# Kernel optimization log

Measured on AMD Instinct MI355X. Metric: run time of the kernel, lower is better.

Reference implementation:

```python
import jax, jax.numpy as jnp
import numpy as np

B, S, R = 8192, 256, 8192  # gas cells, species, reactions


def setup_inputs() -> dict:
    key = jax.random.key(0)
    ks = jax.random.split(key, 10)
    abundances = jax.random.uniform(ks[0], (B, S), jnp.float32, 1e-12, 1.0)
    temperature = jax.random.uniform(ks[1], (B,), jnp.float32, 10.0, 300.0)
    cr_rate = jax.random.uniform(ks[2], (B,), jnp.float32, 0.1, 10.0)
    fuv_rate = jax.random.uniform(ks[3], (B,), jnp.float32, 0.1, 10.0)
    time = jnp.zeros((B,), jnp.float32)  # unused by the RHS, kept for signature parity
    incidence = jax.random.normal(ks[4], (S, R), jnp.float32)  # stoichiometry matrix
    alpha = jax.random.uniform(ks[5], (R,), jnp.float32, 1e-12, 1e-9)
    beta = jax.random.normal(ks[6], (R,), jnp.float32) * 0.5
    gamma = jax.random.uniform(ks[7], (R,), jnp.float32, 0.0, 100.0)
    # species index or S (== out-of-bounds sentinel -> fill_value 1.0, i.e. <2 reactants)
    reactant_multipliers = jax.random.randint(ks[8], (R, 2), 0, S + 1, jnp.int32)
    rtype = jax.random.randint(ks[9], (R,), 0, 3, jnp.int32)  # 0: Arrhenius, 1: CR, 2: FUV
    return {
        'time': time, 'abundances': abundances, 'temperature': temperature,
        'cr_rate': cr_rate, 'fuv_rate': fuv_rate, 'incidence': incidence,
        'alpha': alpha, 'beta': beta, 'gamma': gamma,
        'reactant_multipliers': reactant_multipliers, 'rtype': rtype,
    }


def _get_rates(temperature, cr_rate, fuv_rate, alpha, beta, gamma, rtype):
    # JNetwork.get_rates: hstack of per-reaction rate terms -> (B, R)
    T = temperature[:, None]                                      # (B, 1)
    k_arr = alpha * jnp.exp(beta * jnp.log(T / 300.0) - gamma / T)  # Arrhenius
    k_cr = alpha * cr_rate[:, None]                               # cosmic-ray driven
    k_fuv = alpha * jnp.exp(-gamma) * fuv_rate[:, None]           # FUV photorate
    return jnp.where(rtype == 0, k_arr, jnp.where(rtype == 1, k_cr, k_fuv))


def reference(time, abundances, temperature, cr_rate, fuv_rate,
              incidence, alpha, beta, gamma, reactant_multipliers, rtype):
    rates = _get_rates(temperature, cr_rate, fuv_rate, alpha, beta, gamma, rtype)
    # multiply_rates_by_abundance: gather reactant abundances (mode='drop',
    # fill_value=1.0) and reduce with a product over the 2 reactant slots.
    ones_col = jnp.ones((abundances.shape[0], 1), abundances.dtype)
    ab_pad = jnp.concatenate([abundances, ones_col], axis=1)      # (B, S+1), col S == 1.0
    prod = ab_pad[:, reactant_multipliers[:, 0]] * ab_pad[:, reactant_multipliers[:, 1]]  # (B, R)
    flux = rates * prod                                           # (B, R)
    # incidence @ rates, batched: (S, R) x (B, R) -> (B, S)
    return jnp.einsum('sr,br->bs', incidence, flux)
```

## Files before the change

### kernel.cpp

```cpp
#include <hip/hip_runtime.h>
#include <stdint.h>

typedef __bf16 bf16;
typedef __bf16 bf16x8 __attribute__((ext_vector_type(8)));
typedef float  f32x4  __attribute__((ext_vector_type(4)));

#if __has_builtin(__builtin_amdgcn_exp2f)
#define EXP2F(x) __builtin_amdgcn_exp2f(x)
#else
#define EXP2F(x) exp2f(x)
#endif

#define LGKM_BARRIER()                                    \
  do {                                                    \
    asm volatile("s_waitcnt lgkmcnt(0)" ::: "memory");    \
    __builtin_amdgcn_s_barrier();                         \
  } while (0)

constexpr int Bn = 8192, Sn = 256, Rn = 8192;
constexpr int BM = 64, BK = 32, KP = 4;
constexpr int KLEN = Rn / KP;
constexpr int NC = KLEN / BK;
constexpr int PH = 64;
constexpr int NP = KLEN / PH;

__global__ __launch_bounds__(256) void prep_all(
    const float* __restrict__ inc, bf16* __restrict__ incb,
    const float* __restrict__ alpha, const float* __restrict__ beta,
    const float* __restrict__ gam, const int* __restrict__ rm, const int* __restrict__ rtype,
    float4* __restrict__ params, const float* __restrict__ temp,
    const float* __restrict__ cr, const float* __restrict__ fuv, float4* __restrict__ perb) {
  __shared__ __align__(16) float row_lds[8192];
  __shared__ unsigned short perm_lds[8192];
  __shared__ int c0[256], c1[256], c2[256];
  const int g = blockIdx.x, t = threadIdx.x;

  int* rt = (int*)row_lds;
  {
    const int4* src = (const int4*)rtype;
    int4* dst = (int4*)rt;
#pragma unroll
    for (int i = 0; i < 8; ++i) dst[i * 256 + t] = src[i * 256 + t];
  }
  __syncthreads();

  int ty[32];
  int l0 = 0, l1 = 0, l2 = 0;
#pragma unroll
  for (int i = 0; i < 32; ++i) {
    int v = rt[i * 256 + t];
    ty[i] = v;
    l0 += (v == 0); l1 += (v == 1); l2 += (v == 2);
  }
  c0[t] = l0; c1[t] = l1; c2[t] = l2;
  __syncthreads();
  for (int off = 1; off < 256; off <<= 1) {
    int a = (t >= off) ? c0[t - off] : 0;
    int b = (t >= off) ? c1[t - off] : 0;
    int c = (t >= off) ? c2[t - off] : 0;
    __syncthreads();
    c0[t] += a; c1[t] += b; c2[t] += c;
    __syncthreads();
  }
  const int tot0 = c0[255], tot1 = c1[255];
  int o0 = c0[t] - l0;
  int o1 = tot0 + c1[t] - l1;
  int o2 = tot0 + tot1 + c2[t] - l2;
#pragma unroll
  for (int i = 0; i < 32; ++i) {
    int v = ty[i];
    int pos = (v == 0) ? o0++ : ((v == 1) ? o1++ : o2++);
    perm_lds[pos] = (unsigned short)(i * 256 + t);
  }
  __syncthreads();

  if (g < 32) {
    int p = g * 256 + t;
    int r = perm_lds[p];
    float a = alpha[r], be = beta[r], gm = gam[r];
    int tv = rt[r];
    int i0 = rm[2 * r], i1 = rm[2 * r + 1];
    float x, P = 0.0f, Q = 0.0f;
    if (tv == 0) { x = __log2f(a); P = be; Q = gm; }
    else if (tv == 1) { x = a; }
    else { x = a * expf(-gm); }
    uint32_t bits = (uint32_t)i0 | ((uint32_t)i1 << 10) | ((uint32_t)tv << 20);
    params[p] = make_float4(x, P, Q, __uint_as_float(bits));
  } else if (g < 64) {
    int b = (g - 32) * 256 + t;
    float T = temp[b];
    perb[b] = make_float4(__log2f(T * (1.0f / 300.0f)), 1.4426950408889634f / T,
                          cr[b], fuv[b]);
  }
  __syncthreads();

  {
    const float4* src = (const float4*)(inc + ((size_t)g << 13));
    float4* dst = (float4*)row_lds;
#pragma unroll
    for (int i = 0; i < 8; ++i) dst[i * 256 + t] = src[i * 256 + t];
  }
  __syncthreads();

  const unsigned short* pp = perm_lds + t * 32;
  bf16* outp = incb + ((size_t)t * 256 + g) * 32;
#pragma unroll
  for (int k8 = 0; k8 < 4; ++k8) {
    bf16x8 o;
#pragma unroll
    for (int i = 0; i < 8; ++i) o[i] = (bf16)row_lds[pp[k8 * 8 + i]];
    *(bf16x8*)(outp + k8 * 8) = o;
  }
}

__global__ __launch_bounds__(256, 2) void flux_gemm(
    const float* __restrict__ abund, const float4* __restrict__ perb,
    const float4* __restrict__ params, const bf16* __restrict__ incb,
    float* __restrict__ partial) {
  __shared__ bf16 ab_lds[257 * 64];
  __shared__ bf16 flux_lds[2][64 * PH];

  const int tid  = threadIdx.x;
  const int lane = tid & 63;
  const int w    = tid >> 6;
  const int ws   = __builtin_amdgcn_readfirstlane(w);
  const int x   = blockIdx.x & 7;
  const int jb  = blockIdx.x >> 3;
  const int kp  = x & 3;
  const int m0g = (jb * 2 + (x >> 2)) * BM;
  const int kstart = kp * KLEN;
  const int r16 = lane & 15, q = lane >> 4;

  auto load_params = [&](int ph, float4* pr) {
    const float4* pw = params + kstart + ph * PH + ws * 8;
#pragma unroll
    for (int j = 0; j < 8; ++j) pr[j] = pw[j];
#pragma unroll
    for (int j = 0; j < 8; ++j) pr[8 + j] = pw[32 + j];
  };

  float4 prbuf[16];
  load_params(0, prbuf);

  {
    int bsub = tid >> 2;
    int scol = (tid & 3) * 64;
    const float* rowp = abund + (size_t)(m0g + bsub) * Sn + scol;
#pragma unroll
    for (int j = 0; j < 16; ++j) {
      float4 v = *(const float4*)(rowp + j * 4);
      int s = scol + j * 4;
      ab_lds[(s + 0) * 64 + bsub] = (bf16)v.x;
      ab_lds[(s + 1) * 64 + bsub] = (bf16)v.y;
      ab_lds[(s + 2) * 64 + bsub] = (bf16)v.z;
      ab_lds[(s + 3) * 64 + bsub] = (bf16)v.w;
    }
    if (tid < 64) ab_lds[256 * 64 + tid] = (bf16)1.0f;
  }

  float4 pb = perb[m0g + lane];
  const float l2t = pb.x, nitv = -pb.y, crv = pb.z, fuvv = pb.w;

  auto flux_tile = [&](int buf, int sub, const float4* pr) {
    uint32_t b0 = __builtin_amdgcn_readfirstlane(__float_as_uint(pr[0].w));
    uint32_t b7 = __builtin_amdgcn_readfirstlane(__float_as_uint(pr[7].w));
    uint32_t t0 = b0 >> 20, t7 = b7 >> 20;
    bf16x8 fv;
    if (t0 == 0 && t7 == 0) {
#pragma unroll
      for (int j = 0; j < 8; ++j) {
        uint32_t bits = __builtin_amdgcn_readfirstlane(__float_as_uint(pr[j].w));
        int i0 = (int)(bits & 1023), i1 = (int)((bits >> 10) & 1023);
        float a0 = (float)ab_lds[i0 * 64 + lane];
        float a1 = (float)ab_lds[i1 * 64 + lane];
        float v = EXP2F(fmaf(pr[j].y, l2t, fmaf(pr[j].z, nitv, pr[j].x)));
        fv[j] = (bf16)(v * (a0 * a1));
      }
    } else if (t0 == t7) {
      float mv = (t0 == 1) ? crv : fuvv;
#pragma unroll
      for (int j = 0; j < 8; ++j) {
        uint32_t bits = __builtin_amdgcn_readfirstlane(__float_as_uint(pr[j].w));
        int i0 = (int)(bits & 1023), i1 = (int)((bits >> 10) & 1023);
        float a0 = (float)ab_lds[i0 * 64 + lane];
        float a1 = (float)ab_lds[i1 * 64 + lane];
        fv[j] = (bf16)((pr[j].x * mv) * (a0 * a1));
      }
    } else {
#pragma unroll
      for (int j = 0; j < 8; ++j) {
        uint32_t bits = __builtin_amdgcn_readfirstlane(__float_as_uint(pr[j].w));
        int i0 = (int)(bits & 1023), i1 = (int)((bits >> 10) & 1023), ms = (int)(bits >> 20);
        float a0 = (float)ab_lds[i0 * 64 + lane];
        float a1 = (float)ab_lds[i1 * 64 + lane];
        float ve = EXP2F(fmaf(pr[j].y, l2t, fmaf(pr[j].z, nitv, pr[j].x)));
        float vm = pr[j].x * ((ms == 1) ? crv : fuvv);
        float v = (ms == 0) ? ve : vm;
        fv[j] = (bf16)(v * (a0 * a1));
      }
    }
    *(bf16x8*)(flux_lds[buf] + lane * PH + (((sub * 4 + ws) ^ (lane & 7)) << 3)) = fv;
  };

  const bf16* bbase = incb + (size_t)(kstart / BK) * 8192 + (w * 64 + r16) * BK + q * 8;
  auto load_bfr = [&](int chunk, bf16x8* bfr) {
    const bf16* bp = bbase + (size_t)chunk * 8192;
#pragma unroll
    for (int nt = 0; nt < 4; ++nt)
      bfr[nt] = *(const bf16x8*)(bp + nt * (16 * BK));
  };

  __syncthreads();

  flux_tile(0, 0, prbuf);
  flux_tile(0, 1, prbuf + 8);

  f32x4 acc[4][4];
#pragma unroll
  for (int i = 0; i < 4; ++i)
#pragma unroll
    for (int j = 0; j < 4; ++j) acc[i][j] = (f32x4)0.0f;

  for (int ph = 0; ph < NP; ++ph) {
    const int cur = ph & 1, nxt = cur ^ 1;
    LGKM_BARRIER();

    bf16x8 bfr[2][4];
    load_bfr(ph * 2, bfr[0]);
    load_bfr(ph * 2 + 1, bfr[1]);

    bf16x8 af[2][4];
#pragma unroll
    for (int ks = 0; ks < 2; ++ks)
#pragma unroll
      for (int mt = 0; mt < 4; ++mt) {
        int row = mt * 16 + r16;
        af[ks][mt] = *(const bf16x8*)(flux_lds[cur] + row * PH +
                                      ((((ks << 2) + q) ^ (row & 7)) << 3));
      }

    if (ph + 1 < NP) {
      load_params(ph + 1, prbuf);
      flux_tile(nxt, 0, prbuf);
      flux_tile(nxt, 1, prbuf + 8);
    }

    __builtin_amdgcn_s_setprio(1);
#pragma unroll
    for (int ks = 0; ks < 2; ++ks)
#pragma unroll
      for (int mt = 0; mt < 4; ++mt)
#pragma unroll
        for (int nt = 0; nt < 4; ++nt)
          acc[mt][nt] = __builtin_amdgcn_mfma_f32_16x16x32_bf16(af[ks][mt], bfr[ks][nt],
                                                                acc[mt][nt], 0, 0, 0);
    __builtin_amdgcn_s_setprio(0);
  }

  float* pout = partial + (size_t)kp * Bn * Sn;
#pragma unroll
  for (int mt = 0; mt < 4; ++mt)
#pragma unroll
    for (int nt = 0; nt < 4; ++nt) {
      int col = w * 64 + nt * 16 + r16;
      int row = m0g + mt * 16 + q * 4;
#pragma unroll
      for (int rg = 0; rg < 4; ++rg)
        pout[(size_t)(row + rg) * Sn + col] = acc[mt][nt][rg];
    }
}

__global__ __launch_bounds__(256) void reduce_k(const float* __restrict__ partial,
                                               float* __restrict__ out) {
  size_t i = ((size_t)blockIdx.x * 256 + threadIdx.x) * 4;
  constexpr size_t NS = (size_t)Bn * Sn;
  float4 a = *(const float4*)(partial + i);
  float4 b = *(const float4*)(partial + NS + i);
  float4 c = *(const float4*)(partial + 2 * NS + i);
  float4 d = *(const float4*)(partial + 3 * NS + i);
  float4 r;
  r.x = (a.x + b.x) + (c.x + d.x);
  r.y = (a.y + b.y) + (c.y + d.y);
  r.z = (a.z + b.z) + (c.z + d.z);
  r.w = (a.w + b.w) + (c.w + d.w);
  *(float4*)(out + i) = r;
}

extern "C" void kernel_launch(void* const* d_in, const int* in_sizes, int n_in,
                              void* d_out, int out_size, void* d_ws, size_t ws_size,
                              hipStream_t stream) {
  const float* abund = (const float*)d_in[1];
  const float* temp  = (const float*)d_in[2];
  const float* cr    = (const float*)d_in[3];
  const float* fuv   = (const float*)d_in[4];
  const float* inc   = (const float*)d_in[5];
  const float* alpha = (const float*)d_in[6];
  const float* beta  = (const float*)d_in[7];
  const float* gam   = (const float*)d_in[8];
  const int*   rm    = (const int*)d_in[9];
  const int*   rty   = (const int*)d_in[10];
  float* out = (float*)d_out;

  float4* params  = (float4*)d_ws;
  float4* perb    = params + Rn;
  bf16*   incb    = (bf16*)(perb + Bn);
  float*  partial = (float*)(incb + (size_t)Sn * Rn);

  prep_all<<<256, 256, 0, stream>>>(inc, incb, alpha, beta, gam, rm, rty,
                                    params, temp, cr, fuv, perb);
  flux_gemm<<<(Bn / BM) * KP, 256, 0, stream>>>(abund, perb, params, incb, partial);
  reduce_k<<<(Bn * Sn) / 1024, 256, 0, stream>>>(partial, out);
}
```

Before: 154.8 us.

## Transpose abundances in prep kernel and gather reactants from global memory

The prep kernel gains extra blocks that transpose the abundance matrix to species-major fp32 layout (plus a row of ones for the sentinel index). The GEMM kernel drops its per-block LDS staging of abundances and the initial barrier, and instead gathers reactant abundances directly from the transposed global array with coalesced per-lane loads, batching 16 gathers ahead of the flux math. This removes LDS footprint and staging work, which could raise occupancy. In exchange it adds a global transpose pass and many scattered global/L2 gathers inside the main loop.

```diff
diff --git a/kernel.cpp b/kernel.cpp
--- a/kernel.cpp
+++ b/kernel.cpp
@@ -29,11 +29,39 @@
     const float* __restrict__ alpha, const float* __restrict__ beta,
     const float* __restrict__ gam, const int* __restrict__ rm, const int* __restrict__ rtype,
     float4* __restrict__ params, const float* __restrict__ temp,
-    const float* __restrict__ cr, const float* __restrict__ fuv, float4* __restrict__ perb) {
+    const float* __restrict__ cr, const float* __restrict__ fuv, float4* __restrict__ perb,
+    const float* __restrict__ abund, float* __restrict__ abT) {
   __shared__ __align__(16) float row_lds[8192];
   __shared__ unsigned short perm_lds[8192];
   __shared__ int c0[256], c1[256], c2[256];
   const int g = blockIdx.x, t = threadIdx.x;
+
+  if (g >= 768) {
+    abT[(size_t)Sn * Bn + (size_t)(g - 768) * 256 + t] = 1.0f;
+    return;
+  }
+  if (g >= 256) {
+    const int gg = g - 256;
+    const int bi = gg >> 2, sj = gg & 3;
+    float (*tile)[65] = (float(*)[65])row_lds;
+    const int r0 = t >> 4, c4 = (t & 15) * 4;
+#pragma unroll
+    for (int i = 0; i < 4; ++i) {
+      int r = r0 + i * 16;
+      float4 v = *(const float4*)(abund + (size_t)(bi * 64 + r) * Sn + sj * 64 + c4);
+      tile[r][c4 + 0] = v.x; tile[r][c4 + 1] = v.y;
+      tile[r][c4 + 2] = v.z; tile[r][c4 + 3] = v.w;
+    }
+    __syncthreads();
+#pragma unroll
+    for (int i = 0; i < 4; ++i) {
+      int s = r0 + i * 16;
+      float4 o = make_float4(tile[c4 + 0][s], tile[c4 + 1][s],
+                             tile[c4 + 2][s], tile[c4 + 3][s]);
+      *(float4*)(abT + (size_t)(sj * 64 + s) * Bn + bi * 64 + c4) = o;
+    }
+    return;
+  }
 
   int* rt = (int*)row_lds;
   {
@@ -114,10 +142,9 @@
 }
 
 __global__ __launch_bounds__(256, 2) void flux_gemm(
-    const float* __restrict__ abund, const float4* __restrict__ perb,
+    const float* __restrict__ abT, const float4* __restrict__ perb,
     const float4* __restrict__ params, const bf16* __restrict__ incb,
     float* __restrict__ partial) {
-  __shared__ bf16 ab_lds[257 * 64];
   __shared__ bf16 flux_lds[2][64 * PH];
 
   const int tid  = threadIdx.x;
@@ -131,6 +158,8 @@
   const int kstart = kp * KLEN;
   const int r16 = lane & 15, q = lane >> 4;
 
+  const float* abTb = abT + m0g + lane;
+
   auto load_params = [&](int ph, float4* pr) {
     const float4* pw = params + kstart + ph * PH + ws * 8;
 #pragma unroll
@@ -142,64 +171,51 @@
   float4 prbuf[16];
   load_params(0, prbuf);
 
-  {
-    int bsub = tid >> 2;
-    int scol = (tid & 3) * 64;
-    const float* rowp = abund + (size_t)(m0g + bsub) * Sn + scol;
-#pragma unroll
-    for (int j = 0; j < 16; ++j) {
-      float4 v = *(const float4*)(rowp + j * 4);
-      int s = scol + j * 4;
-      ab_lds[(s + 0) * 64 + bsub] = (bf16)v.x;
-      ab_lds[(s + 1) * 64 + bsub] = (bf16)v.y;
-      ab_lds[(s + 2) * 64 + bsub] = (bf16)v.z;
-      ab_lds[(s + 3) * 64 + bsub] = (bf16)v.w;
-    }
-    if (tid < 64) ab_lds[256 * 64 + tid] = (bf16)1.0f;
-  }
-
   float4 pb = perb[m0g + lane];
   const float l2t = pb.x, nitv = -pb.y, crv = pb.z, fuvv = pb.w;
 
-  auto flux_tile = [&](int buf, int sub, const float4* pr) {
-    uint32_t b0 = __builtin_amdgcn_readfirstlane(__float_as_uint(pr[0].w));
-    uint32_t b7 = __builtin_amdgcn_readfirstlane(__float_as_uint(pr[7].w));
-    uint32_t t0 = b0 >> 20, t7 = b7 >> 20;
-    bf16x8 fv;
-    if (t0 == 0 && t7 == 0) {
-#pragma unroll
-      for (int j = 0; j < 8; ++j) {
-        uint32_t bits = __builtin_amdgcn_readfirstlane(__float_as_uint(pr[j].w));
-        int i0 = (int)(bits & 1023), i1 = (int)((bits >> 10) & 1023);
-        float a0 = (float)ab_lds[i0 * 64 + lane];
-        float a1 = (float)ab_lds[i1 * 64 + lane];
-        float v = EXP2F(fmaf(pr[j].y, l2t, fmaf(pr[j].z, nitv, pr[j].x)));
-        fv[j] = (bf16)(v * (a0 * a1));
+  auto flux_tile = [&](int buf, const float4* pr) {
+    float a0v[16], a1v[16];
+#pragma unroll
+    for (int j = 0; j < 16; ++j) {
+      uint32_t bits = __builtin_amdgcn_readfirstlane(__float_as_uint(pr[j].w));
+      int i0 = (int)(bits & 1023), i1 = (int)((bits >> 10) & 1023);
+      a0v[j] = abTb[(size_t)i0 * Bn];
+      a1v[j] = abTb[(size_t)i1 * Bn];
+    }
+#pragma unroll
+    for (int sub = 0; sub < 2; ++sub) {
+      const float4* prs = pr + sub * 8;
+      const float* A0 = a0v + sub * 8;
+      const float* A1 = a1v + sub * 8;
+      uint32_t b0 = __builtin_amdgcn_readfirstlane(__float_as_uint(prs[0].w));
+      uint32_t b7 = __builtin_amdgcn_readfirstlane(__float_as_uint(prs[7].w));
+      uint32_t t0 = b0 >> 20, t7 = b7 >> 20;
+      bf16x8 fv;
+      if (t0 == 0 && t7 == 0) {
+#pragma unroll
+        for (int j = 0; j < 8; ++j) {
+          float v = EXP2F(fmaf(prs[j].y, l2t, fmaf(prs[j].z, nitv, prs[j].x)));
+          fv[j] = (bf16)(v * (A0[j] * A1[j]));
+        }
+      } else if (t0 == t7) {
+        float mv = (t0 == 1) ? crv : fuvv;
+#pragma unroll
+        for (int j = 0; j < 8; ++j)
+          fv[j] = (bf16)((prs[j].x * mv) * (A0[j] * A1[j]));
+      } else {
+#pragma unroll
+        for (int j = 0; j < 8; ++j) {
+          uint32_t bits = __builtin_amdgcn_readfirstlane(__float_as_uint(prs[j].w));
+          int ms = (int)(bits >> 20);
+          float ve = EXP2F(fmaf(prs[j].y, l2t, fmaf(prs[j].z, nitv, prs[j].x)));
+          float vm = prs[j].x * ((ms == 1) ? crv : fuvv);
+          float v = (ms == 0) ? ve : vm;
+          fv[j] = (bf16)(v * (A0[j] * A1[j]));
+        }
       }
-    } else if (t0 == t7) {
-      float mv = (t0 == 1) ? crv : fuvv;
-#pragma unroll
-      for (int j = 0; j < 8; ++j) {
-        uint32_t bits = __builtin_amdgcn_readfirstlane(__float_as_uint(pr[j].w));
-        int i0 = (int)(bits & 1023), i1 = (int)((bits >> 10) & 1023);
-        float a0 = (float)ab_lds[i0 * 64 + lane];
-        float a1 = (float)ab_lds[i1 * 64 + lane];
-        fv[j] = (bf16)((pr[j].x * mv) * (a0 * a1));
-      }
-    } else {
-#pragma unroll
-      for (int j = 0; j < 8; ++j) {
-        uint32_t bits = __builtin_amdgcn_readfirstlane(__float_as_uint(pr[j].w));
-        int i0 = (int)(bits & 1023), i1 = (int)((bits >> 10) & 1023), ms = (int)(bits >> 20);
-        float a0 = (float)ab_lds[i0 * 64 + lane];
-        float a1 = (float)ab_lds[i1 * 64 + lane];
-        float ve = EXP2F(fmaf(pr[j].y, l2t, fmaf(pr[j].z, nitv, pr[j].x)));
-        float vm = pr[j].x * ((ms == 1) ? crv : fuvv);
-        float v = (ms == 0) ? ve : vm;
-        fv[j] = (bf16)(v * (a0 * a1));
-      }
-    }
-    *(bf16x8*)(flux_lds[buf] + lane * PH + (((sub * 4 + ws) ^ (lane & 7)) << 3)) = fv;
+      *(bf16x8*)(flux_lds[buf] + lane * PH + (((sub * 4 + ws) ^ (lane & 7)) << 3)) = fv;
+    }
   };
 
   const bf16* bbase = incb + (size_t)(kstart / BK) * 8192 + (w * 64 + r16) * BK + q * 8;
@@ -210,10 +226,7 @@
       bfr[nt] = *(const bf16x8*)(bp + nt * (16 * BK));
   };
 
-  __syncthreads();
-
-  flux_tile(0, 0, prbuf);
-  flux_tile(0, 1, prbuf + 8);
+  flux_tile(0, prbuf);
 
   f32x4 acc[4][4];
 #pragma unroll
@@ -241,8 +254,7 @@
 
     if (ph + 1 < NP) {
       load_params(ph + 1, prbuf);
-      flux_tile(nxt, 0, prbuf);
-      flux_tile(nxt, 1, prbuf + 8);
+      flux_tile(nxt, prbuf);
     }
 
     __builtin_amdgcn_s_setprio(1);
@@ -304,10 +316,11 @@
   float4* params  = (float4*)d_ws;
   float4* perb    = params + Rn;
   bf16*   incb    = (bf16*)(perb + Bn);
-  float*  partial = (float*)(incb + (size_t)Sn * Rn);
-
-  prep_all<<<256, 256, 0, stream>>>(inc, incb, alpha, beta, gam, rm, rty,
-                                    params, temp, cr, fuv, perb);
-  flux_gemm<<<(Bn / BM) * KP, 256, 0, stream>>>(abund, perb, params, incb, partial);
+  float*  abT     = (float*)(incb + (size_t)Sn * Rn);
+  float*  partial = abT + (size_t)(Sn + 1) * Bn;
+
+  prep_all<<<800, 256, 0, stream>>>(inc, incb, alpha, beta, gam, rm, rty,
+                                    params, temp, cr, fuv, perb, abund, abT);
+  flux_gemm<<<(Bn / BM) * KP, 256, 0, stream>>>(abT, perb, params, incb, partial);
   reduce_k<<<(Bn * Sn) / 1024, 256, 0, stream>>>(partial, out);
 }
```

Measured after the change: 164.1 us. +6.0%, slower.

## Use 512-thread blocks with 2x4 wave grid in flux GEMM

Applied to the files above, without the earlier changes.

Doubles threads per block to 8 waves arranged as 2 (M) by 4 (N), so each wave computes a 32x64 output tile instead of 64x64 and produces one flux sub-tile per phase instead of two. Parameter loads move inside the flux tile routine, which removes the 16-entry prefetch register buffer. The aim is lower per-wave register use and more waves per CU to hide latency. In exchange, each wave reloads the B fragments for a smaller M tile, which adds redundant global/L2 traffic, and there is more barrier cost per block.

```diff
diff --git a/kernel.cpp b/kernel.cpp
--- a/kernel.cpp
+++ b/kernel.cpp
@@ -20,7 +20,6 @@
 constexpr int Bn = 8192, Sn = 256, Rn = 8192;
 constexpr int BM = 64, BK = 32, KP = 4;
 constexpr int KLEN = Rn / KP;
-constexpr int NC = KLEN / BK;
 constexpr int PH = 64;
 constexpr int NP = KLEN / PH;
 
@@ -113,7 +112,7 @@
   }
 }
 
-__global__ __launch_bounds__(256, 2) void flux_gemm(
+__global__ __launch_bounds__(512, 4) void flux_gemm(
     const float* __restrict__ abund, const float4* __restrict__ perb,
     const float4* __restrict__ params, const bf16* __restrict__ incb,
     float* __restrict__ partial) {
@@ -124,6 +123,8 @@
   const int lane = tid & 63;
   const int w    = tid >> 6;
   const int ws   = __builtin_amdgcn_readfirstlane(w);
+  const int wm   = ws >> 2;
+  const int wn   = ws & 3;
   const int x   = blockIdx.x & 7;
   const int jb  = blockIdx.x >> 3;
   const int kp  = x & 3;
@@ -131,23 +132,12 @@
   const int kstart = kp * KLEN;
   const int r16 = lane & 15, q = lane >> 4;
 
-  auto load_params = [&](int ph, float4* pr) {
-    const float4* pw = params + kstart + ph * PH + ws * 8;
-#pragma unroll
-    for (int j = 0; j < 8; ++j) pr[j] = pw[j];
-#pragma unroll
-    for (int j = 0; j < 8; ++j) pr[8 + j] = pw[32 + j];
-  };
-
-  float4 prbuf[16];
-  load_params(0, prbuf);
-
   {
-    int bsub = tid >> 2;
-    int scol = (tid & 3) * 64;
+    int bsub = tid >> 3;
+    int scol = (tid & 7) * 32;
     const float* rowp = abund + (size_t)(m0g + bsub) * Sn + scol;
 #pragma unroll
-    for (int j = 0; j < 16; ++j) {
+    for (int j = 0; j < 8; ++j) {
       float4 v = *(const float4*)(rowp + j * 4);
       int s = scol + j * 4;
       ab_lds[(s + 0) * 64 + bsub] = (bf16)v.x;
@@ -161,7 +151,11 @@
   float4 pb = perb[m0g + lane];
   const float l2t = pb.x, nitv = -pb.y, crv = pb.z, fuvv = pb.w;
 
-  auto flux_tile = [&](int buf, int sub, const float4* pr) {
+  auto flux_tile = [&](int buf, int kb) {
+    const float4* pw = params + kb + ws * 8;
+    float4 pr[8];
+#pragma unroll
+    for (int j = 0; j < 8; ++j) pr[j] = pw[j];
     uint32_t b0 = __builtin_amdgcn_readfirstlane(__float_as_uint(pr[0].w));
     uint32_t b7 = __builtin_amdgcn_readfirstlane(__float_as_uint(pr[7].w));
     uint32_t t0 = b0 >> 20, t7 = b7 >> 20;
@@ -199,10 +193,10 @@
         fv[j] = (bf16)(v * (a0 * a1));
       }
     }
-    *(bf16x8*)(flux_lds[buf] + lane * PH + (((sub * 4 + ws) ^ (lane & 7)) << 3)) = fv;
+    *(bf16x8*)(flux_lds[buf] + lane * PH + ((ws ^ (lane & 7)) << 3)) = fv;
   };
 
-  const bf16* bbase = incb + (size_t)(kstart / BK) * 8192 + (w * 64 + r16) * BK + q * 8;
+  const bf16* bbase = incb + (size_t)(kstart / BK) * 8192 + (wn * 64 + r16) * BK + q * 8;
   auto load_bfr = [&](int chunk, bf16x8* bfr) {
     const bf16* bp = bbase + (size_t)chunk * 8192;
 #pragma unroll
@@ -212,12 +206,11 @@
 
   __syncthreads();
 
-  flux_tile(0, 0, prbuf);
-  flux_tile(0, 1, prbuf + 8);
-
-  f32x4 acc[4][4];
-#pragma unroll
-  for (int i = 0; i < 4; ++i)
+  flux_tile(0, kstart);
+
+  f32x4 acc[2][4];
+#pragma unroll
+  for (int i = 0; i < 2; ++i)
 #pragma unroll
     for (int j = 0; j < 4; ++j) acc[i][j] = (f32x4)0.0f;
 
@@ -229,27 +222,23 @@
     load_bfr(ph * 2, bfr[0]);
     load_bfr(ph * 2 + 1, bfr[1]);
 
-    bf16x8 af[2][4];
+    bf16x8 af[2][2];
 #pragma unroll
     for (int ks = 0; ks < 2; ++ks)
 #pragma unroll
-      for (int mt = 0; mt < 4; ++mt) {
-        int row = mt * 16 + r16;
+      for (int mt = 0; mt < 2; ++mt) {
+        int row = wm * 32 + mt * 16 + r16;
         af[ks][mt] = *(const bf16x8*)(flux_lds[cur] + row * PH +
                                       ((((ks << 2) + q) ^ (row & 7)) << 3));
       }
 
-    if (ph + 1 < NP) {
-      load_params(ph + 1, prbuf);
-      flux_tile(nxt, 0, prbuf);
-      flux_tile(nxt, 1, prbuf + 8);
-    }
+    if (ph + 1 < NP) flux_tile(nxt, kstart + (ph + 1) * PH);
 
     __builtin_amdgcn_s_setprio(1);
 #pragma unroll
     for (int ks = 0; ks < 2; ++ks)
 #pragma unroll
-      for (int mt = 0; mt < 4; ++mt)
+      for (int mt = 0; mt < 2; ++mt)
 #pragma unroll
         for (int nt = 0; nt < 4; ++nt)
           acc[mt][nt] = __builtin_amdgcn_mfma_f32_16x16x32_bf16(af[ks][mt], bfr[ks][nt],
@@ -259,11 +248,11 @@
 
   float* pout = partial + (size_t)kp * Bn * Sn;
 #pragma unroll
-  for (int mt = 0; mt < 4; ++mt)
+  for (int mt = 0; mt < 2; ++mt)
 #pragma unroll
     for (int nt = 0; nt < 4; ++nt) {
-      int col = w * 64 + nt * 16 + r16;
-      int row = m0g + mt * 16 + q * 4;
+      int col = wn * 64 + nt * 16 + r16;
+      int row = m0g + wm * 32 + mt * 16 + q * 4;
 #pragma unroll
       for (int rg = 0; rg < 4; ++rg)
         pout[(size_t)(row + rg) * Sn + col] = acc[mt][nt][rg];
@@ -308,6 +297,6 @@
 
   prep_all<<<256, 256, 0, stream>>>(inc, incb, alpha, beta, gam, rm, rty,
                                     params, temp, cr, fuv, perb);
-  flux_gemm<<<(Bn / BM) * KP, 256, 0, stream>>>(abund, perb, params, incb, partial);
+  flux_gemm<<<(Bn / BM) * KP, 512, 0, stream>>>(abund, perb, params, incb, partial);
   reduce_k<<<(Bn * Sn) / 1024, 256, 0, stream>>>(partial, out);
 }
```

New measurement: 168.1 us. 8.6% more time.
